# Kernel tuning notes

Measured on AMD Instinct MI355X. Metric: run time of the kernel, lower is better.

The kernel has to match this reference:

```python
import jax, jax.numpy as jnp
import numpy as np

L = 262144      # number of points
C = 256         # in_channels
NH = 8          # num_heads
G = 64          # group_size
FF = 2048       # torch TransformerEncoderLayer default dim_feedforward
LPAD = 262144   # padded length, divisible by G; LPAD//G divisible by batch_size
BS = 4


def setup_inputs() -> dict:
    key = jax.random.key(0)
    ks = jax.random.split(key, 12)
    def w(k, shape, scale=0.02):
        return jax.random.normal(k, shape, jnp.float32) * scale
    return {
        "feats_flat": jax.random.normal(ks[0], (L, C), jnp.float32),
        "x_idx": jax.random.randint(ks[1], (L,), 0, L),
        "flat2win": jax.random.randint(ks[2], (LPAD,), 0, L),
        "win2flat": jax.random.randint(ks[3], (L,), 0, LPAD),
        "in_proj_w": w(ks[4], (3 * C, C)),
        "in_proj_b": jnp.zeros((3 * C,), jnp.float32),
        "out_proj_w": w(ks[5], (C, C)),
        "out_proj_b": jnp.zeros((C,), jnp.float32),
        "lin1_w": w(ks[6], (FF, C)),
        "lin1_b": jnp.zeros((FF,), jnp.float32),
        "lin2_w": w(ks[7], (C, FF)),
        "lin2_b": jnp.zeros((C,), jnp.float32),
        "ln1_g": jnp.ones((C,), jnp.float32),
        "ln1_b": jnp.zeros((C,), jnp.float32),
        "ln2_g": jnp.ones((C,), jnp.float32),
        "ln2_b": jnp.zeros((C,), jnp.float32),
        "proj_w": w(ks[8], (C, 2 * C)),
        "proj_b": jnp.zeros((C,), jnp.float32),
        "batch_size": BS,
    }


def _layer_norm(x, g, b, eps=1e-5):
    mu = jnp.mean(x, axis=-1, keepdims=True)
    var = jnp.var(x, axis=-1, keepdims=True)
    return (x - mu) * jax.lax.rsqrt(var + eps) * g + b


def _mha(x, in_proj_w, in_proj_b, out_proj_w, out_proj_b):
    B, S, Cm = x.shape
    hd = Cm // NH
    qkv = x @ in_proj_w.T + in_proj_b                      # [B,S,3C]
    q, k, v = jnp.split(qkv, 3, axis=-1)
    q = q.reshape(B, S, NH, hd)
    k = k.reshape(B, S, NH, hd)
    v = v.reshape(B, S, NH, hd)
    scores = jnp.einsum("bqhd,bkhd->bhqk", q, k) / jnp.sqrt(jnp.float32(hd))
    attn = jax.nn.softmax(scores, axis=-1)
    out = jnp.einsum("bhqk,bkhd->bqhd", attn, v).reshape(B, S, Cm)
    return out @ out_proj_w.T + out_proj_b


def reference(feats_flat, x_idx, flat2win, win2flat,
              in_proj_w, in_proj_b, out_proj_w, out_proj_b,
              lin1_w, lin1_b, lin2_w, lin2_b,
              ln1_g, ln1_b, ln2_g, ln2_b,
              proj_w, proj_b, batch_size):
    Cc = feats_flat.shape[1]
    # gather: feats_flat[indices][flat2win] -> [NW, G, C]
    feats_win = feats_flat[x_idx][flat2win].reshape(-1, G, Cc)
    # adaptive max pool over the group axis -> [NW, C]
    feats_pool = jnp.max(feats_win, axis=1)
    # torch TransformerEncoderLayer (post-norm, relu, eval/no-dropout)
    x = feats_pool.reshape(batch_size, -1, Cc)             # [B, S, C]
    x = _layer_norm(x + _mha(x, in_proj_w, in_proj_b, out_proj_w, out_proj_b), ln1_g, ln1_b)
    ff = jax.nn.relu(x @ lin1_w.T + lin1_b) @ lin2_w.T + lin2_b
    x = _layer_norm(x + ff, ln2_g, ln2_b)
    feats_global = x.reshape(-1, Cc)                       # [NW, C]
    # broadcast global feature to every group element, concat (global first)
    fuse_in = jnp.concatenate(
        [jnp.broadcast_to(feats_global[:, None, :], feats_win.shape), feats_win],
        axis=-1)                                           # [NW, G, 2C]
    feats_fuse = (fuse_in @ proj_w.T + proj_b).reshape(-1, Cc)  # [LPAD, C]
    # scatter back: feats_flat[indices] = feats_fuse[win2flat]
    return feats_flat.at[x_idx].set(feats_fuse[win2flat])
```

## Files before the change

### kernel.cpp

```cpp
#include <hip/hip_runtime.h>
#include <math.h>

namespace {
constexpr int kL    = 262144;
constexpr int kC    = 256;
constexpr int kNH   = 8;
constexpr int kG    = 64;
constexpr int kFF   = 2048;
constexpr int kLPAD = 262144;
constexpr int kBS   = 4;
constexpr int kNW   = kLPAD / kG;
constexpr int kS    = kNW / kBS;
constexpr int kHD   = kC / kNH;

constexpr size_t MB        = 1024 * 1024;
constexpr size_t OFF_GIDX   = 0;
constexpr size_t OFF_WINNER = 1 * MB;
constexpr size_t OFF_WLIST  = 2 * MB;
constexpr size_t OFF_CNT    = 3 * MB;
constexpr size_t OFF_X0     = 4 * MB;
constexpr size_t OFF_BASE   = 8 * MB;
constexpr size_t OFF_ATTN   = 12 * MB;
constexpr size_t OFF_QH     = 16 * MB;
constexpr size_t OFF_KH     = 18 * MB;
constexpr size_t OFF_VH     = 20 * MB;
constexpr size_t OFF_X1     = 24 * MB;
constexpr size_t OFF_FF1    = 32 * MB;
constexpr size_t OFF_WINB   = 64 * MB;
constexpr size_t OFF_WOUTB  = OFF_WINB  + 512 * 1024;
constexpr size_t OFF_W1B    = OFF_WOUTB + 256 * 1024;
constexpr size_t OFF_W2B    = OFF_W1B   + 1536 * 1024;
constexpr size_t OFF_WP1B   = OFF_W2B   + 1536 * 1024;
constexpr size_t OFF_WP2B   = OFF_WP1B  + 256 * 1024;

typedef __attribute__((ext_vector_type(8))) short bf16x8;
typedef __attribute__((ext_vector_type(4))) float f32x4;

__device__ inline unsigned short f2bf(float f) {
  union { float f; unsigned int u; } x; x.f = f;
  unsigned int r = x.u + 0x7fff + ((x.u >> 16) & 1);
  return (unsigned short)(r >> 16);
}
}

__global__ __launch_bounds__(256) void k_winner(const int* __restrict__ x_idx,
                                                int* __restrict__ winner) {
  int i = blockIdx.x * 256 + threadIdx.x;
  atomicMax(&winner[x_idx[i]], i);
}

__global__ __launch_bounds__(256) void k_compact(const int* __restrict__ x_idx,
                                                 const int* __restrict__ winner,
                                                 int* __restrict__ wlist,
                                                 int* __restrict__ cnt) {
  int i = blockIdx.x * 256 + threadIdx.x;
  if (winner[x_idx[i]] == i) {
    int p = atomicAdd(cnt, 1);
    wlist[p] = i;
  }
}

__global__ __launch_bounds__(256) void k_copy(const float* __restrict__ feats,
                                              const int* __restrict__ winner,
                                              float* __restrict__ out) {
  size_t idx = (size_t)blockIdx.x * 256 + threadIdx.x;
  int row = (int)(idx >> 6);
  int c4 = (int)(idx & 63);
  if (winner[row] < 0) {
    *(float4*)&out[(size_t)row * kC + c4 * 4] =
        *(const float4*)&feats[(size_t)row * kC + c4 * 4];
  }
}

__global__ __launch_bounds__(256) void k_pool(const float* __restrict__ feats,
                                              const int* __restrict__ x_idx,
                                              const int* __restrict__ flat2win,
                                              int* __restrict__ gidx,
                                              float* __restrict__ x0) {
  int w = blockIdx.x, t = threadIdx.x;
  __shared__ int rows[kG];
  if (t < kG) {
    int g = x_idx[flat2win[w * kG + t]];
    rows[t] = g;
    gidx[w * kG + t] = g;
  }
  __syncthreads();
  float m = -INFINITY;
  #pragma unroll 4
  for (int g = 0; g < kG; ++g)
    m = fmaxf(m, feats[(size_t)rows[g] * kC + t]);
  x0[w * kC + t] = m;
}

__global__ __launch_bounds__(256) void k_wcast(const float* __restrict__ in_proj_w,
                                               const float* __restrict__ out_proj_w,
                                               const float* __restrict__ lin1_w,
                                               const float* __restrict__ lin2_w,
                                               const float* __restrict__ proj_w,
                                               unsigned short* __restrict__ WINB,
                                               unsigned short* __restrict__ WOUTB,
                                               unsigned short* __restrict__ W1B,
                                               unsigned short* __restrict__ W2B,
                                               unsigned short* __restrict__ WP1,
                                               unsigned short* __restrict__ WP2) {
  int blk = blockIdx.x, t = threadIdx.x;
  const float* src = nullptr; unsigned short* dst = nullptr; int i = 0;
  if (blk < 192)       { src = in_proj_w;  dst = WINB;  i = blk * 256 + t; }
  else if (blk < 256)  { src = out_proj_w; dst = WOUTB; i = (blk - 192) * 256 + t; }
  else if (blk < 768)  { src = lin1_w;     dst = W1B;   i = (blk - 256) * 256 + t; }
  else if (blk < 1280) { src = lin2_w;     dst = W2B;   i = (blk - 768) * 256 + t; }
  else {
    int c = blk - 1280;
    WP1[c * kC + t] = f2bf(proj_w[(size_t)c * (2 * kC) + t]);
    WP2[c * kC + t] = f2bf(proj_w[(size_t)c * (2 * kC) + kC + t]);
    return;
  }
  float4 v = ((const float4*)src)[i];
  ushort4 b;
  b.x = f2bf(v.x); b.y = f2bf(v.y); b.z = f2bf(v.z); b.w = f2bf(v.w);
  ((ushort4*)dst)[i] = b;
}

__global__ __launch_bounds__(256) void k_gemm_qkv(const float* __restrict__ A,
                                                  const unsigned short* __restrict__ Wb,
                                                  const float* __restrict__ bias,
                                                  unsigned short* __restrict__ Qh,
                                                  unsigned short* __restrict__ Kh,
                                                  unsigned short* __restrict__ Vh) {
  const float scale = 0.17677669529663687f;
  const int m0 = blockIdx.y * 64;
  const int sec = blockIdx.x;
  const int t = threadIdx.x;
  const int lane = t & 63, w = t >> 6;
  const int c0 = w * 64;
  const int kb = lane >> 4, lr = lane & 15;

  __shared__ __align__(16) unsigned short As[64 * 256];

  f32x4 acc[4][4] = {};
  #pragma unroll
  for (int i = 0; i < 16; ++i) {
    int row = i * 4 + w;
    float4 f4 = *(const float4*)&A[(size_t)(m0 + row) * kC + lane * 4];
    ushort4 b4;
    b4.x = f2bf(f4.x); b4.y = f2bf(f4.y); b4.z = f2bf(f4.z); b4.w = f2bf(f4.w);
    unsigned int off = (((unsigned)row * 512u) + (unsigned)lane * 8u) ^ (((unsigned)row & 7u) << 4);
    *(ushort4*)((char*)As + off) = b4;
  }
  __syncthreads();

  #pragma unroll
  for (int ks = 0; ks < 8; ++ks) {
    const int k0 = ks * 32;
    bf16x8 a[4], b[4];
    #pragma unroll
    for (int rt = 0; rt < 4; ++rt) {
      int row = rt * 16 + lr;
      unsigned int off = (((unsigned)row * 512u) + (unsigned)(k0 + kb * 8) * 2u) ^
                         (((unsigned)row & 7u) << 4);
      a[rt] = *(const bf16x8*)((const char*)As + off);
    }
    #pragma unroll
    for (int ct = 0; ct < 4; ++ct) {
      int c = sec * kC + c0 + ct * 16 + lr;
      b[ct] = *(const bf16x8*)&Wb[(size_t)c * kC + k0 + kb * 8];
    }
    #pragma unroll
    for (int rt = 0; rt < 4; ++rt)
      #pragma unroll
      for (int ct = 0; ct < 4; ++ct)
        acc[rt][ct] = __builtin_amdgcn_mfma_f32_16x16x32_bf16(a[rt], b[ct], acc[rt][ct], 0, 0, 0);
  }

  unsigned short* dstbuf = (sec == 0) ? Qh : (sec == 1) ? Kh : Vh;
  #pragma unroll
  for (int rt = 0; rt < 4; ++rt) {
    #pragma unroll
    for (int r = 0; r < 4; ++r) {
      int row = m0 + rt * 16 + kb * 4 + r;
      int bb = row >> 10, s = row & 1023;
      #pragma unroll
      for (int ct = 0; ct < 4; ++ct) {
        int c = c0 + ct * 16 + lr;
        float v = acc[rt][ct][r] + bias[sec * kC + c];
        if (sec == 0) v *= scale;
        int h = c >> 5, d = c & 31;
        dstbuf[(((size_t)(bb * kNH + h) * kS) + s) * kHD + d] = f2bf(v);
      }
    }
  }
}

__global__ __launch_bounds__(256) void k_attn(const unsigned short* __restrict__ Qh,
                                              const unsigned short* __restrict__ Kh,
                                              const unsigned short* __restrict__ Vh,
                                              unsigned short* __restrict__ attn_out) {
  const int q0 = blockIdx.x * 64;
  const int bh = blockIdx.y;
  const int b = bh >> 3, h = bh & 7;
  const int t = threadIdx.x;
  const int lane = t & 63, w = t >> 6;
  const int kb = lane >> 4, lr = lane & 15;

  __shared__ __align__(16) unsigned short Ks[64][40];
  __shared__ __align__(16) unsigned short VTs[32][72];
  __shared__ __align__(16) unsigned short Ps[4][16][72];

  bf16x8 aq = *(const bf16x8*)(Qh + (((size_t)bh * kS) + q0 + w * 16 + lr) * kHD + kb * 8);

  const unsigned short* kbase = Kh + (size_t)bh * kS * kHD;
  const unsigned short* vbase = Vh + (size_t)bh * kS * kHD;

  float m[4], l[4];
  f32x4 O[2] = {};
  #pragma unroll
  for (int r = 0; r < 4; ++r) { m[r] = -INFINITY; l[r] = 0.f; }

  for (int kt = 0; kt < kS / 64; ++kt) {
    {
      int key = t >> 2, d0 = (t & 3) * 8;
      size_t srow = ((size_t)(kt * 64 + key)) * kHD + d0;
      bf16x8 kv = *(const bf16x8*)(kbase + srow);
      *(bf16x8*)&Ks[key][d0] = kv;
      bf16x8 vv = *(const bf16x8*)(vbase + srow);
      #pragma unroll
      for (int i = 0; i < 8; ++i) VTs[d0 + i][key] = (unsigned short)vv[i];
    }
    __syncthreads();

    f32x4 S[4] = {};
    #pragma unroll
    for (int ct = 0; ct < 4; ++ct) {
      bf16x8 bk = *(const bf16x8*)&Ks[ct * 16 + lr][kb * 8];
      S[ct] = __builtin_amdgcn_mfma_f32_16x16x32_bf16(aq, bk, S[ct], 0, 0, 0);
    }

    float alpha[4];
    #pragma unroll
    for (int r = 0; r < 4; ++r) {
      float tmax = fmaxf(fmaxf(S[0][r], S[1][r]), fmaxf(S[2][r], S[3][r]));
      #pragma unroll
      for (int off = 8; off; off >>= 1) tmax = fmaxf(tmax, __shfl_xor(tmax, off, 16));
      float newm = fmaxf(m[r], tmax);
      alpha[r] = __expf(m[r] - newm);
      float p[4], ps = 0.f;
      #pragma unroll
      for (int ct = 0; ct < 4; ++ct) { p[ct] = __expf(S[ct][r] - newm); ps += p[ct]; }
      #pragma unroll
      for (int off = 8; off; off >>= 1) ps += __shfl_xor(ps, off, 16);
      l[r] = l[r] * alpha[r] + ps;
      m[r] = newm;
      #pragma unroll
      for (int ct = 0; ct < 4; ++ct) Ps[w][kb * 4 + r][ct * 16 + lr] = f2bf(p[ct]);
    }
    #pragma unroll
    for (int r = 0; r < 4; ++r) { O[0][r] *= alpha[r]; O[1][r] *= alpha[r]; }

    #pragma unroll
    for (int ks = 0; ks < 2; ++ks) {
      bf16x8 ap = *(const bf16x8*)&Ps[w][lr][ks * 32 + kb * 8];
      #pragma unroll
      for (int ct = 0; ct < 2; ++ct) {
        bf16x8 bv = *(const bf16x8*)&VTs[ct * 16 + lr][ks * 32 + kb * 8];
        O[ct] = __builtin_amdgcn_mfma_f32_16x16x32_bf16(ap, bv, O[ct], 0, 0, 0);
      }
    }
    __syncthreads();
  }

  #pragma unroll
  for (int ct = 0; ct < 2; ++ct) {
    #pragma unroll
    for (int r = 0; r < 4; ++r) {
      size_t row = (size_t)b * kS + q0 + w * 16 + kb * 4 + r;
      attn_out[row * kC + h * kHD + ct * 16 + lr] = f2bf(O[ct][r] / l[r]);
    }
  }
}

template <bool DO_BASE>
__global__ __launch_bounds__(256) void k_gemm_ln(const unsigned short* __restrict__ A,
                                                 int K,
                                                 const unsigned short* __restrict__ Wb,
                                                 const float* __restrict__ bias,
                                                 const float* __restrict__ R,
                                                 const float* __restrict__ g,
                                                 const float* __restrict__ bb,
                                                 float* __restrict__ Out,
                                                 const unsigned short* __restrict__ WbB,
                                                 const float* __restrict__ biasB) {
  const int m0 = blockIdx.x * 16;
  const int t = threadIdx.x;
  const int lane = t & 63, w = t >> 6;
  const int c0 = w * 64;
  const int kb = lane >> 4, lr = lane & 15;

  __shared__ __align__(16) unsigned short As[16 * 256];
  __shared__ __align__(16) unsigned short Xs[16 * 256];
  __shared__ float red[2][16][4];

  f32x4 acc[4] = {};
  for (int kc = 0; kc < K; kc += 256) {
    #pragma unroll
    for (int i = 0; i < 2; ++i) {
      int idx = i * 256 + t;
      int row = idx >> 5, seg = idx & 31;
      bf16x8 v = *(const bf16x8*)&A[(size_t)(m0 + row) * K + kc + seg * 8];
      unsigned int off = (((unsigned)row * 512u) + (unsigned)seg * 16u) ^ (((unsigned)row & 7u) << 4);
      *(bf16x8*)((char*)As + off) = v;
    }
    __syncthreads();

    #pragma unroll
    for (int ks = 0; ks < 8; ++ks) {
      const int k0 = ks * 32;
      unsigned int aoff = (((unsigned)lr * 512u) + (unsigned)(k0 + kb * 8) * 2u) ^
                          (((unsigned)lr & 7u) << 4);
      bf16x8 a = *(const bf16x8*)((const char*)As + aoff);
      #pragma unroll
      for (int ct = 0; ct < 4; ++ct) {
        bf16x8 b = *(const bf16x8*)&Wb[(size_t)(c0 + ct * 16 + lr) * K + kc + k0 + kb * 8];
        acc[ct] = __builtin_amdgcn_mfma_f32_16x16x32_bf16(a, b, acc[ct], 0, 0, 0);
      }
    }
    __syncthreads();
  }

  float v[4][4];
  float s[4], sq[4];
  #pragma unroll
  for (int r = 0; r < 4; ++r) { s[r] = 0.f; sq[r] = 0.f; }
  #pragma unroll
  for (int r = 0; r < 4; ++r) {
    int row = m0 + kb * 4 + r;
    #pragma unroll
    for (int ct = 0; ct < 4; ++ct) {
      int c = c0 + ct * 16 + lr;
      float x = acc[ct][r] + bias[c] + R[(size_t)row * kC + c];
      v[r][ct] = x;
      s[r] += x;
      sq[r] += x * x;
    }
  }
  #pragma unroll
  for (int r = 0; r < 4; ++r) {
    #pragma unroll
    for (int off = 8; off; off >>= 1) {
      s[r]  += __shfl_xor(s[r], off, 16);
      sq[r] += __shfl_xor(sq[r], off, 16);
    }
    if (lr == 0) { red[0][kb * 4 + r][w] = s[r]; red[1][kb * 4 + r][w] = sq[r]; }
  }
  __syncthreads();

  #pragma unroll
  for (int r = 0; r < 4; ++r) {
    int lrow = kb * 4 + r;
    float su = red[0][lrow][0] + red[0][lrow][1] + red[0][lrow][2] + red[0][lrow][3];
    float sg = red[1][lrow][0] + red[1][lrow][1] + red[1][lrow][2] + red[1][lrow][3];
    float mu = su * (1.0f / kC);
    float var = sg * (1.0f / kC) - mu * mu;
    float rs = rsqrtf(var + 1e-5f);
    #pragma unroll
    for (int ct = 0; ct < 4; ++ct) {
      int c = c0 + ct * 16 + lr;
      float yv = (v[r][ct] - mu) * rs * g[c] + bb[c];
      if (!DO_BASE) {
        Out[(size_t)(m0 + lrow) * kC + c] = yv;
      } else {
        unsigned int off = (((unsigned)lrow * 512u) + (unsigned)c * 2u) ^ (((unsigned)lrow & 7u) << 4);
        *(unsigned short*)((char*)Xs + off) = f2bf(yv);
      }
    }
  }

  if (DO_BASE) {
    __syncthreads();
    f32x4 acc2[4] = {};
    #pragma unroll
    for (int ks = 0; ks < 8; ++ks) {
      const int k0 = ks * 32;
      unsigned int aoff = (((unsigned)lr * 512u) + (unsigned)(k0 + kb * 8) * 2u) ^
                          (((unsigned)lr & 7u) << 4);
      bf16x8 a = *(const bf16x8*)((const char*)Xs + aoff);
      #pragma unroll
      for (int ct = 0; ct < 4; ++ct) {
        bf16x8 b = *(const bf16x8*)&WbB[(size_t)(c0 + ct * 16 + lr) * kC + k0 + kb * 8];
        acc2[ct] = __builtin_amdgcn_mfma_f32_16x16x32_bf16(a, b, acc2[ct], 0, 0, 0);
      }
    }
    #pragma unroll
    for (int r = 0; r < 4; ++r) {
      int row = m0 + kb * 4 + r;
      #pragma unroll
      for (int ct = 0; ct < 4; ++ct) {
        int c = c0 + ct * 16 + lr;
        Out[(size_t)row * kC + c] = acc2[ct][r] + biasB[c];
      }
    }
  }
}

__global__ __launch_bounds__(256) void k_gemm_ff1(const float* __restrict__ A,
                                                  const unsigned short* __restrict__ Wb,
                                                  const float* __restrict__ bias,
                                                  unsigned short* __restrict__ Cc) {
  const int m0 = blockIdx.y * 64;
  const int nb = blockIdx.x * 256;
  const int t = threadIdx.x;
  const int lane = t & 63, w = t >> 6;
  const int c0 = nb + w * 64;
  const int kb = lane >> 4, lr = lane & 15;

  __shared__ __align__(16) unsigned short As[64 * 256];

  f32x4 acc[4][4] = {};
  #pragma unroll
  for (int i = 0; i < 16; ++i) {
    int row = i * 4 + w;
    float4 f4 = *(const float4*)&A[(size_t)(m0 + row) * kC + lane * 4];
    ushort4 b4;
    b4.x = f2bf(f4.x); b4.y = f2bf(f4.y); b4.z = f2bf(f4.z); b4.w = f2bf(f4.w);
    unsigned int off = (((unsigned)row * 512u) + (unsigned)lane * 8u) ^ (((unsigned)row & 7u) << 4);
    *(ushort4*)((char*)As + off) = b4;
  }
  __syncthreads();

  #pragma unroll
  for (int ks = 0; ks < 8; ++ks) {
    const int k0 = ks * 32;
    bf16x8 a[4], b[4];
    #pragma unroll
    for (int rt = 0; rt < 4; ++rt) {
      int row = rt * 16 + lr;
      unsigned int off = (((unsigned)row * 512u) + (unsigned)(k0 + kb * 8) * 2u) ^
                         (((unsigned)row & 7u) << 4);
      a[rt] = *(const bf16x8*)((const char*)As + off);
    }
    #pragma unroll
    for (int ct = 0; ct < 4; ++ct) {
      int c = c0 + ct * 16 + lr;
      b[ct] = *(const bf16x8*)&Wb[(size_t)c * kC + k0 + kb * 8];
    }
    #pragma unroll
    for (int rt = 0; rt < 4; ++rt)
      #pragma unroll
      for (int ct = 0; ct < 4; ++ct)
        acc[rt][ct] = __builtin_amdgcn_mfma_f32_16x16x32_bf16(a[rt], b[ct], acc[rt][ct], 0, 0, 0);
  }

  #pragma unroll
  for (int rt = 0; rt < 4; ++rt) {
    #pragma unroll
    for (int r = 0; r < 4; ++r) {
      int row = m0 + rt * 16 + kb * 4 + r;
      #pragma unroll
      for (int ct = 0; ct < 4; ++ct) {
        int c = c0 + ct * 16 + lr;
        float vv = fmaxf(acc[rt][ct][r] + bias[c], 0.f);
        Cc[(size_t)row * kFF + c] = f2bf(vv);
      }
    }
  }
}

__global__ __launch_bounds__(256) void k_fuse(const float* __restrict__ feats,
                                              const int* __restrict__ gidx,
                                              const int* __restrict__ wlist,
                                              const int* __restrict__ cnt,
                                              const int* __restrict__ win2flat,
                                              const int* __restrict__ x_idx,
                                              const float* __restrict__ base,
                                              const unsigned short* __restrict__ W2B,
                                              float* __restrict__ out) {
  const int count = cnt[0];
  const int r0 = blockIdx.x * 64;
  if (r0 >= count) return;
  const int nr = min(64, count - r0);
  const int t = threadIdx.x;
  const int lane = t & 63, w = t >> 6;

  __shared__ __align__(16) unsigned short As[64 * 256];
  __shared__ int dstrow[64], wwin[64], srcrow[64];

  if (t < 64) {
    int rr = min(r0 + t, count - 1);
    int i = wlist[rr];
    int j = win2flat[i];
    srcrow[t] = gidx[j];
    wwin[t] = j >> 6;
    dstrow[t] = x_idx[i];
  }
  __syncthreads();

  for (int i = 0; i < 16; ++i) {
    int row = i * 4 + w;
    float4 f4 = *(const float4*)&feats[(size_t)srcrow[row] * kC + lane * 4];
    ushort4 b4;
    b4.x = f2bf(f4.x); b4.y = f2bf(f4.y); b4.z = f2bf(f4.z); b4.w = f2bf(f4.w);
    unsigned int off = (((unsigned)row * 512u) + (unsigned)lane * 8u) ^ (((unsigned)row & 7u) << 4);
    *(ushort4*)((char*)As + off) = b4;
  }
  __syncthreads();

  const int c0 = w * 64;
  const int kb = lane >> 4;
  const int lr = lane & 15;
  f32x4 acc[4][4] = {};
  for (int ks = 0; ks < 8; ++ks) {
    const int k0 = ks * 32;
    bf16x8 a[4], b[4];
    #pragma unroll
    for (int rt = 0; rt < 4; ++rt) {
      int row = rt * 16 + lr;
      unsigned int off = (((unsigned)row * 512u) + (unsigned)(k0 + kb * 8) * 2u) ^
                         (((unsigned)row & 7u) << 4);
      a[rt] = *(const bf16x8*)((const char*)As + off);
    }
    #pragma unroll
    for (int ct = 0; ct < 4; ++ct) {
      int c = c0 + ct * 16 + lr;
      b[ct] = *(const bf16x8*)&W2B[(size_t)c * kC + k0 + kb * 8];
    }
    #pragma unroll
    for (int rt = 0; rt < 4; ++rt)
      #pragma unroll
      for (int ct = 0; ct < 4; ++ct)
        acc[rt][ct] = __builtin_amdgcn_mfma_f32_16x16x32_bf16(a[rt], b[ct], acc[rt][ct], 0, 0, 0);
  }

  #pragma unroll
  for (int rt = 0; rt < 4; ++rt) {
    #pragma unroll
    for (int r = 0; r < 4; ++r) {
      int row = rt * 16 + kb * 4 + r;
      if (row < nr) {
        size_t orow = (size_t)dstrow[row] * kC;
        size_t brow = (size_t)wwin[row] * kC;
        #pragma unroll
        for (int ct = 0; ct < 4; ++ct) {
          int c = c0 + ct * 16 + lr;
          out[orow + c] = acc[rt][ct][r] + base[brow + c];
        }
      }
    }
  }
}

extern "C" void kernel_launch(void* const* d_in, const int* in_sizes, int n_in,
                              void* d_out, int out_size, void* d_ws, size_t ws_size,
                              hipStream_t stream) {
  const float* feats      = (const float*)d_in[0];
  const int*   x_idx      = (const int*)d_in[1];
  const int*   flat2win   = (const int*)d_in[2];
  const int*   win2flat   = (const int*)d_in[3];
  const float* in_proj_w  = (const float*)d_in[4];
  const float* in_proj_b  = (const float*)d_in[5];
  const float* out_proj_w = (const float*)d_in[6];
  const float* out_proj_b = (const float*)d_in[7];
  const float* lin1_w     = (const float*)d_in[8];
  const float* lin1_b     = (const float*)d_in[9];
  const float* lin2_w     = (const float*)d_in[10];
  const float* lin2_b     = (const float*)d_in[11];
  const float* ln1_g      = (const float*)d_in[12];
  const float* ln1_b      = (const float*)d_in[13];
  const float* ln2_g      = (const float*)d_in[14];
  const float* ln2_b      = (const float*)d_in[15];
  const float* proj_w     = (const float*)d_in[16];
  const float* proj_b     = (const float*)d_in[17];

  char* ws = (char*)d_ws;
  int*   gidx   = (int*)(ws + OFF_GIDX);
  int*   winner = (int*)(ws + OFF_WINNER);
  int*   wlist  = (int*)(ws + OFF_WLIST);
  int*   cnt    = (int*)(ws + OFF_CNT);
  float* x0     = (float*)(ws + OFF_X0);
  float* basep  = (float*)(ws + OFF_BASE);
  float* x1     = (float*)(ws + OFF_X1);
  unsigned short* attnb = (unsigned short*)(ws + OFF_ATTN);
  unsigned short* Qh    = (unsigned short*)(ws + OFF_QH);
  unsigned short* Kh    = (unsigned short*)(ws + OFF_KH);
  unsigned short* Vh    = (unsigned short*)(ws + OFF_VH);
  unsigned short* ff1b  = (unsigned short*)(ws + OFF_FF1);
  unsigned short* WINB  = (unsigned short*)(ws + OFF_WINB);
  unsigned short* WOUTB = (unsigned short*)(ws + OFF_WOUTB);
  unsigned short* W1B   = (unsigned short*)(ws + OFF_W1B);
  unsigned short* W2B   = (unsigned short*)(ws + OFF_W2B);
  unsigned short* WP1B  = (unsigned short*)(ws + OFF_WP1B);
  unsigned short* WP2B  = (unsigned short*)(ws + OFF_WP2B);
  float* out    = (float*)d_out;

  hipMemsetAsync(winner, 0xFF, (size_t)kL * sizeof(int), stream);
  hipMemsetAsync(cnt, 0, sizeof(int), stream);

  k_winner<<<kL / 256, 256, 0, stream>>>(x_idx, winner);
  k_compact<<<kL / 256, 256, 0, stream>>>(x_idx, winner, wlist, cnt);
  k_copy<<<kL / 4, 256, 0, stream>>>(feats, winner, out);
  k_pool<<<kNW, 256, 0, stream>>>(feats, x_idx, flat2win, gidx, x0);
  k_wcast<<<1536, 256, 0, stream>>>(in_proj_w, out_proj_w, lin1_w, lin2_w, proj_w,
                                    WINB, WOUTB, W1B, W2B, WP1B, WP2B);

  k_gemm_qkv<<<dim3(3, kNW / 64), 256, 0, stream>>>(x0, WINB, in_proj_b, Qh, Kh, Vh);
  k_attn<<<dim3(kS / 64, kBS * kNH), 256, 0, stream>>>(Qh, Kh, Vh, attnb);
  k_gemm_ln<false><<<kNW / 16, 256, 0, stream>>>(
      attnb, kC, WOUTB, out_proj_b, x0, ln1_g, ln1_b, x1, nullptr, nullptr);
  k_gemm_ff1<<<dim3(kFF / 256, kNW / 64), 256, 0, stream>>>(x1, W1B, lin1_b, ff1b);
  k_gemm_ln<true><<<kNW / 16, 256, 0, stream>>>(
      ff1b, kFF, W2B, lin2_b, x1, ln2_g, ln2_b, basep, WP1B, proj_b);
  k_fuse<<<kL / 64, 256, 0, stream>>>(feats, gidx, wlist, cnt, win2flat, x_idx,
                                      basep, WP2B, out);
}
```

Baseline: 404.1 us.

## Merge small prologue kernels and widen attention key tile to 128

Folds the counter reset into k_winner, merges the compaction and weight-cast kernels into one launch, and merges pooling with the passthrough copy into another. This removes one memset and two launches. Separately, the attention kernel now processes 128 keys per iteration instead of 64, halving loop trips and barriers. The cost is more LDS and registers per block, which may lower occupancy.

```diff
diff --git a/kernel.cpp b/kernel.cpp
--- a/kernel.cpp
+++ b/kernel.cpp
@@ -44,81 +44,85 @@
 }
 
 __global__ __launch_bounds__(256) void k_winner(const int* __restrict__ x_idx,
-                                                int* __restrict__ winner) {
+                                                int* __restrict__ winner,
+                                                int* __restrict__ cnt) {
   int i = blockIdx.x * 256 + threadIdx.x;
+  if (i == 0) cnt[0] = 0;
   atomicMax(&winner[x_idx[i]], i);
 }
 
-__global__ __launch_bounds__(256) void k_compact(const int* __restrict__ x_idx,
-                                                 const int* __restrict__ winner,
-                                                 int* __restrict__ wlist,
-                                                 int* __restrict__ cnt) {
-  int i = blockIdx.x * 256 + threadIdx.x;
-  if (winner[x_idx[i]] == i) {
-    int p = atomicAdd(cnt, 1);
-    wlist[p] = i;
-  }
-}
-
-__global__ __launch_bounds__(256) void k_copy(const float* __restrict__ feats,
-                                              const int* __restrict__ winner,
-                                              float* __restrict__ out) {
-  size_t idx = (size_t)blockIdx.x * 256 + threadIdx.x;
+__global__ __launch_bounds__(256) void k_fc(const int* __restrict__ x_idx,
+                                            const int* __restrict__ winner,
+                                            int* __restrict__ wlist,
+                                            int* __restrict__ cnt,
+                                            const float* __restrict__ in_proj_w,
+                                            const float* __restrict__ out_proj_w,
+                                            const float* __restrict__ lin1_w,
+                                            const float* __restrict__ lin2_w,
+                                            const float* __restrict__ proj_w,
+                                            unsigned short* __restrict__ WINB,
+                                            unsigned short* __restrict__ WOUTB,
+                                            unsigned short* __restrict__ W1B,
+                                            unsigned short* __restrict__ W2B,
+                                            unsigned short* __restrict__ WP1,
+                                            unsigned short* __restrict__ WP2) {
+  int blk = blockIdx.x, t = threadIdx.x;
+  if (blk < 1024) {
+    int i = blk * 256 + t;
+    if (winner[x_idx[i]] == i) {
+      int p = atomicAdd(cnt, 1);
+      wlist[p] = i;
+    }
+    return;
+  }
+  int b2 = blk - 1024;
+  const float* src = nullptr; unsigned short* dst = nullptr; int i = 0;
+  if (b2 < 192)       { src = in_proj_w;  dst = WINB;  i = b2 * 256 + t; }
+  else if (b2 < 256)  { src = out_proj_w; dst = WOUTB; i = (b2 - 192) * 256 + t; }
+  else if (b2 < 768)  { src = lin1_w;     dst = W1B;   i = (b2 - 256) * 256 + t; }
+  else if (b2 < 1280) { src = lin2_w;     dst = W2B;   i = (b2 - 768) * 256 + t; }
+  else {
+    int c = b2 - 1280;
+    WP1[c * kC + t] = f2bf(proj_w[(size_t)c * (2 * kC) + t]);
+    WP2[c * kC + t] = f2bf(proj_w[(size_t)c * (2 * kC) + kC + t]);
+    return;
+  }
+  float4 v = ((const float4*)src)[i];
+  ushort4 b;
+  b.x = f2bf(v.x); b.y = f2bf(v.y); b.z = f2bf(v.z); b.w = f2bf(v.w);
+  ((ushort4*)dst)[i] = b;
+}
+
+__global__ __launch_bounds__(256) void k_pc(const float* __restrict__ feats,
+                                            const int* __restrict__ x_idx,
+                                            const int* __restrict__ flat2win,
+                                            const int* __restrict__ winner,
+                                            int* __restrict__ gidx,
+                                            float* __restrict__ x0,
+                                            float* __restrict__ out) {
+  int blk = blockIdx.x, t = threadIdx.x;
+  if (blk < kNW) {
+    __shared__ int rows[kG];
+    if (t < kG) {
+      int g = x_idx[flat2win[blk * kG + t]];
+      rows[t] = g;
+      gidx[blk * kG + t] = g;
+    }
+    __syncthreads();
+    float m = -INFINITY;
+    #pragma unroll 4
+    for (int g = 0; g < kG; ++g)
+      m = fmaxf(m, feats[(size_t)rows[g] * kC + t]);
+    x0[blk * kC + t] = m;
+    return;
+  }
+  size_t idx = (size_t)(blk - kNW) * 256 + t;
   int row = (int)(idx >> 6);
   int c4 = (int)(idx & 63);
   if (winner[row] < 0) {
     *(float4*)&out[(size_t)row * kC + c4 * 4] =
         *(const float4*)&feats[(size_t)row * kC + c4 * 4];
   }
-}
-
-__global__ __launch_bounds__(256) void k_pool(const float* __restrict__ feats,
-                                              const int* __restrict__ x_idx,
-                                              const int* __restrict__ flat2win,
-                                              int* __restrict__ gidx,
-                                              float* __restrict__ x0) {
-  int w = blockIdx.x, t = threadIdx.x;
-  __shared__ int rows[kG];
-  if (t < kG) {
-    int g = x_idx[flat2win[w * kG + t]];
-    rows[t] = g;
-    gidx[w * kG + t] = g;
-  }
-  __syncthreads();
-  float m = -INFINITY;
-  #pragma unroll 4
-  for (int g = 0; g < kG; ++g)
-    m = fmaxf(m, feats[(size_t)rows[g] * kC + t]);
-  x0[w * kC + t] = m;
-}
-
-__global__ __launch_bounds__(256) void k_wcast(const float* __restrict__ in_proj_w,
-                                               const float* __restrict__ out_proj_w,
-                                               const float* __restrict__ lin1_w,
-                                               const float* __restrict__ lin2_w,
-                                               const float* __restrict__ proj_w,
-                                               unsigned short* __restrict__ WINB,
-                                               unsigned short* __restrict__ WOUTB,
-                                               unsigned short* __restrict__ W1B,
-                                               unsigned short* __restrict__ W2B,
-                                               unsigned short* __restrict__ WP1,
-                                               unsigned short* __restrict__ WP2) {
-  int blk = blockIdx.x, t = threadIdx.x;
-  const float* src = nullptr; unsigned short* dst = nullptr; int i = 0;
-  if (blk < 192)       { src = in_proj_w;  dst = WINB;  i = blk * 256 + t; }
-  else if (blk < 256)  { src = out_proj_w; dst = WOUTB; i = (blk - 192) * 256 + t; }
-  else if (blk < 768)  { src = lin1_w;     dst = W1B;   i = (blk - 256) * 256 + t; }
-  else if (blk < 1280) { src = lin2_w;     dst = W2B;   i = (blk - 768) * 256 + t; }
-  else {
-    int c = blk - 1280;
-    WP1[c * kC + t] = f2bf(proj_w[(size_t)c * (2 * kC) + t]);
-    WP2[c * kC + t] = f2bf(proj_w[(size_t)c * (2 * kC) + kC + t]);
-    return;
-  }
-  float4 v = ((const float4*)src)[i];
-  ushort4 b;
-  b.x = f2bf(v.x); b.y = f2bf(v.y); b.z = f2bf(v.z); b.w = f2bf(v.w);
-  ((ushort4*)dst)[i] = b;
 }
 
 __global__ __launch_bounds__(256) void k_gemm_qkv(const float* __restrict__ A,
@@ -202,9 +206,9 @@
   const int lane = t & 63, w = t >> 6;
   const int kb = lane >> 4, lr = lane & 15;
 
-  __shared__ __align__(16) unsigned short Ks[64][40];
-  __shared__ __align__(16) unsigned short VTs[32][72];
-  __shared__ __align__(16) unsigned short Ps[4][16][72];
+  __shared__ __align__(16) unsigned short Ks[128][40];
+  __shared__ __align__(16) unsigned short VTs[32][136];
+  __shared__ __align__(16) unsigned short Ps[4][16][136];
 
   bf16x8 aq = *(const bf16x8*)(Qh + (((size_t)bh * kS) + q0 + w * 16 + lr) * kHD + kb * 8);
 
@@ -216,21 +220,27 @@
   #pragma unroll
   for (int r = 0; r < 4; ++r) { m[r] = -INFINITY; l[r] = 0.f; }
 
-  for (int kt = 0; kt < kS / 64; ++kt) {
+  for (int kt = 0; kt < kS / 128; ++kt) {
     {
-      int key = t >> 2, d0 = (t & 3) * 8;
-      size_t srow = ((size_t)(kt * 64 + key)) * kHD + d0;
-      bf16x8 kv = *(const bf16x8*)(kbase + srow);
-      *(bf16x8*)&Ks[key][d0] = kv;
-      bf16x8 vv = *(const bf16x8*)(vbase + srow);
-      #pragma unroll
-      for (int i = 0; i < 8; ++i) VTs[d0 + i][key] = (unsigned short)vv[i];
+      int key = t >> 1, d0 = (t & 1) * 16;
+      size_t srow = ((size_t)(kt * 128 + key)) * kHD + d0;
+      bf16x8 kv0 = *(const bf16x8*)(kbase + srow);
+      bf16x8 kv1 = *(const bf16x8*)(kbase + srow + 8);
+      *(bf16x8*)&Ks[key][d0] = kv0;
+      *(bf16x8*)&Ks[key][d0 + 8] = kv1;
+      bf16x8 vv0 = *(const bf16x8*)(vbase + srow);
+      bf16x8 vv1 = *(const bf16x8*)(vbase + srow + 8);
+      #pragma unroll
+      for (int i = 0; i < 8; ++i) {
+        VTs[d0 + i][key] = (unsigned short)vv0[i];
+        VTs[d0 + 8 + i][key] = (unsigned short)vv1[i];
+      }
     }
     __syncthreads();
 
-    f32x4 S[4] = {};
-    #pragma unroll
-    for (int ct = 0; ct < 4; ++ct) {
+    f32x4 S[8] = {};
+    #pragma unroll
+    for (int ct = 0; ct < 8; ++ct) {
       bf16x8 bk = *(const bf16x8*)&Ks[ct * 16 + lr][kb * 8];
       S[ct] = __builtin_amdgcn_mfma_f32_16x16x32_bf16(aq, bk, S[ct], 0, 0, 0);
     }
@@ -238,26 +248,30 @@
     float alpha[4];
     #pragma unroll
     for (int r = 0; r < 4; ++r) {
-      float tmax = fmaxf(fmaxf(S[0][r], S[1][r]), fmaxf(S[2][r], S[3][r]));
+      float tmax = -INFINITY;
+      #pragma unroll
+      for (int ct = 0; ct < 8; ++ct) tmax = fmaxf(tmax, S[ct][r]);
       #pragma unroll
       for (int off = 8; off; off >>= 1) tmax = fmaxf(tmax, __shfl_xor(tmax, off, 16));
       float newm = fmaxf(m[r], tmax);
       alpha[r] = __expf(m[r] - newm);
-      float p[4], ps = 0.f;
-      #pragma unroll
-      for (int ct = 0; ct < 4; ++ct) { p[ct] = __expf(S[ct][r] - newm); ps += p[ct]; }
+      float ps = 0.f;
+      #pragma unroll
+      for (int ct = 0; ct < 8; ++ct) {
+        float p = __expf(S[ct][r] - newm);
+        ps += p;
+        Ps[w][kb * 4 + r][ct * 16 + lr] = f2bf(p);
+      }
       #pragma unroll
       for (int off = 8; off; off >>= 1) ps += __shfl_xor(ps, off, 16);
       l[r] = l[r] * alpha[r] + ps;
       m[r] = newm;
-      #pragma unroll
-      for (int ct = 0; ct < 4; ++ct) Ps[w][kb * 4 + r][ct * 16 + lr] = f2bf(p[ct]);
     }
     #pragma unroll
     for (int r = 0; r < 4; ++r) { O[0][r] *= alpha[r]; O[1][r] *= alpha[r]; }
 
     #pragma unroll
-    for (int ks = 0; ks < 2; ++ks) {
+    for (int ks = 0; ks < 4; ++ks) {
       bf16x8 ap = *(const bf16x8*)&Ps[w][lr][ks * 32 + kb * 8];
       #pragma unroll
       for (int ct = 0; ct < 2; ++ct) {
@@ -591,14 +605,12 @@
   float* out    = (float*)d_out;
 
   hipMemsetAsync(winner, 0xFF, (size_t)kL * sizeof(int), stream);
-  hipMemsetAsync(cnt, 0, sizeof(int), stream);
-
-  k_winner<<<kL / 256, 256, 0, stream>>>(x_idx, winner);
-  k_compact<<<kL / 256, 256, 0, stream>>>(x_idx, winner, wlist, cnt);
-  k_copy<<<kL / 4, 256, 0, stream>>>(feats, winner, out);
-  k_pool<<<kNW, 256, 0, stream>>>(feats, x_idx, flat2win, gidx, x0);
-  k_wcast<<<1536, 256, 0, stream>>>(in_proj_w, out_proj_w, lin1_w, lin2_w, proj_w,
-                                    WINB, WOUTB, W1B, W2B, WP1B, WP2B);
+
+  k_winner<<<kL / 256, 256, 0, stream>>>(x_idx, winner, cnt);
+  k_fc<<<1024 + 1536, 256, 0, stream>>>(x_idx, winner, wlist, cnt,
+                                        in_proj_w, out_proj_w, lin1_w, lin2_w, proj_w,
+                                        WINB, WOUTB, W1B, W2B, WP1B, WP2B);
+  k_pc<<<kNW + kL / 4, 256, 0, stream>>>(feats, x_idx, flat2win, winner, gidx, x0, out);
 
   k_gemm_qkv<<<dim3(3, kNW / 64), 256, 0, stream>>>(x0, WINB, in_proj_b, Qh, Kh, Vh);
   k_attn<<<dim3(kS / 64, kBS * kNH), 256, 0, stream>>>(Qh, Kh, Vh, attnb);
```

Result: faster. 385.8 us (-4.5%).
